# Optimization experiments

Hardware: AMD Instinct MI355X
Metric: run time of the kernel (lower is better)

Reference implementation:

```python
import jax, jax.numpy as jnp
import numpy as np

N_NODES = 20000
N_EDGES = 640000
NODE_DIM = 128
EDGE_DIM = 64
HID = 128  # must equal NODE_DIM (index_add_ into zeros_like(node_feat) in the original)
EPS = 1e-8


def setup_inputs() -> dict:
    key = jax.random.key(0)
    ks = jax.random.split(key, 16)
    s = 0.05
    return {
        "node_feat": jax.random.normal(ks[0], (N_NODES, NODE_DIM), jnp.float32),
        "edge_index": jax.random.randint(ks[1], (2, N_EDGES), 0, N_NODES, jnp.int32),
        "edge_attr": jax.random.normal(ks[2], (N_EDGES, EDGE_DIM), jnp.float32),
        "coords": jax.random.normal(ks[3], (N_NODES, 3), jnp.float32),
        # edge_mlp: Linear(2*node+edge -> hid), SiLU, Linear(hid -> hid), SiLU
        "eW1": jax.random.normal(ks[4], (2 * NODE_DIM + EDGE_DIM, HID), jnp.float32) * s,
        "eb1": jnp.zeros((HID,), jnp.float32),
        "eW2": jax.random.normal(ks[5], (HID, HID), jnp.float32) * s,
        "eb2": jnp.zeros((HID,), jnp.float32),
        # node_mlp: Linear(node+hid -> hid), SiLU, Linear(hid -> node)
        "nW1": jax.random.normal(ks[6], (NODE_DIM + HID, HID), jnp.float32) * s,
        "nb1": jnp.zeros((HID,), jnp.float32),
        "nW2": jax.random.normal(ks[7], (HID, NODE_DIM), jnp.float32) * s,
        "nb2": jnp.zeros((NODE_DIM,), jnp.float32),
        # coord_mlp: Linear(hid -> hid//2), SiLU, Linear(hid//2 -> 1)
        "cW1": jax.random.normal(ks[8], (HID, HID // 2), jnp.float32) * s,
        "cb1": jnp.zeros((HID // 2,), jnp.float32),
        "cW2": jax.random.normal(ks[9], (HID // 2, 1), jnp.float32) * s,
        "cb2": jnp.zeros((1,), jnp.float32),
    }


def reference(node_feat, edge_index, edge_attr, coords,
              eW1, eb1, eW2, eb2, nW1, nb1, nW2, nb2, cW1, cb1, cW2, cb2):
    silu = jax.nn.silu
    src, dst = edge_index[0], edge_index[1]

    # edge messages: gather -> concat -> 2-layer MLP (SiLU after both layers)
    edge_feat = jnp.concatenate([node_feat[src], node_feat[dst], edge_attr], axis=-1)  # [E, 2*node+edge]
    edge_message = silu(silu(edge_feat @ eW1 + eb1) @ eW2 + eb2)  # [E, hid]

    # aggregate messages per destination node (index_add_)
    aggr_message = jax.ops.segment_sum(edge_message, dst, num_segments=N_NODES)  # [N, hid]

    # node update (residual)
    node_input = jnp.concatenate([node_feat, aggr_message], axis=-1)
    node_update = silu(node_input @ nW1 + nb1) @ nW2 + nb2
    updated_nodes = node_feat + node_update

    # coordinate update: per-edge scalar weight times unit direction, scattered to dst
    coord_weights = silu(edge_message @ cW1 + cb1) @ cW2 + cb2  # [E, 1]
    coord_diff = coords[src] - coords[dst]  # [E, 3]
    coord_diff = coord_diff / (jnp.linalg.norm(coord_diff, axis=-1, keepdims=True) + EPS)
    coord_update = jax.ops.segment_sum(coord_weights * coord_diff, dst, num_segments=N_NODES)
    updated_coords = coords + coord_update

    return updated_nodes, updated_coords
```

## Files before the change

kernel.cpp:

```cpp
#include <hip/hip_runtime.h>
#include <math.h>

#define N_NODES 20000
#define N_EDGES 640000
#define D 128
#define ED 64
#define EPS 1e-8f
#define MT 64

#define FSTRIDE 328
#define HSTRIDE 136
#define MSG_OFF (MT * HSTRIDE)
#define LDS_SHORTS (MT * FSTRIDE)

#define NSTRIDE 264

#define EW2_OFF 40960
#define CW1_OFF 57344
#define NW1_OFF 65536
#define NW2_OFF 98304
#define NFBF_OFF 114688
#define CSR_OFF  2674688

typedef __attribute__((ext_vector_type(8))) short bf16x8;
typedef __attribute__((ext_vector_type(4))) short bf16x4;
typedef __attribute__((ext_vector_type(16))) float f32x16;

__device__ __forceinline__ float silu_f(float x) { return x / (1.0f + __expf(-x)); }

__device__ __forceinline__ short f2bf(float f) {
    union { float f; unsigned u; } v; v.f = f;
    unsigned r = v.u + 0x7FFFu + ((v.u >> 16) & 1u);
    return (short)(r >> 16);
}
__device__ __forceinline__ float bf2f(short s) {
    union { unsigned u; float f; } v;
    v.u = ((unsigned)(unsigned short)s) << 16;
    return v.f;
}

#define SWZ_ADD(x, imm) (x + __int_as_float( \
    __builtin_amdgcn_ds_swizzle(__float_as_int(x), imm)))

__global__ __launch_bounds__(256)
void prep_kernel(const float* __restrict__ eW1, const float* __restrict__ eW2,
                 const float* __restrict__ cW1, const float* __restrict__ nW1,
                 const float* __restrict__ nW2,
                 const float* __restrict__ node_feat,
                 const float* __restrict__ coords,
                 short* __restrict__ wsf, short* __restrict__ nfbf,
                 int* __restrict__ cnt,
                 float* __restrict__ nodes_io, float* __restrict__ out_coords) {
    const int t = blockIdx.x * blockDim.x + threadIdx.x;
    const int nthr = gridDim.x * blockDim.x;

    if (t < 224 * 64) {
        int f = t >> 6, lane = t & 63;
        const float* src; int kc, nt, ncol; size_t dst;
        if (f < 80)       {              src = eW1; kc = f >> 2;  nt = f & 3;  ncol = 128; dst = (size_t)f * 512; }
        else if (f < 112) { int g=f-80;  src = eW2; kc = g >> 2;  nt = g & 3;  ncol = 128; dst = EW2_OFF + (size_t)g * 512; }
        else if (f < 128) { int g=f-112; src = cW1; kc = g >> 1;  nt = g & 1;  ncol = 64;  dst = CW1_OFF + (size_t)g * 512; }
        else if (f < 192) { int g=f-128; src = nW1; kc = g >> 2;  nt = g & 3;  ncol = 128; dst = NW1_OFF + (size_t)g * 512; }
        else              { int g=f-192; src = nW2; kc = g >> 2;  nt = g & 3;  ncol = 128; dst = NW2_OFF + (size_t)g * 512; }
        int col = nt * 32 + (lane & 31);
        int k0  = kc * 16 + (lane >> 5) * 8;
        bf16x8 o;
        #pragma unroll
        for (int j = 0; j < 8; ++j) o[j] = f2bf(src[(size_t)(k0 + j) * ncol + col]);
        *(bf16x8*)&wsf[dst + (size_t)lane * 8] = o;
    }
    for (int idx = t; idx < N_NODES * D / 8; idx += nthr) {
        const float* s = node_feat + (size_t)idx * 8;
        float4 f0 = *(const float4*)s, f1 = *(const float4*)(s + 4);
        bf16x8 pk;
        pk[0]=f2bf(f0.x); pk[1]=f2bf(f0.y); pk[2]=f2bf(f0.z); pk[3]=f2bf(f0.w);
        pk[4]=f2bf(f1.x); pk[5]=f2bf(f1.y); pk[6]=f2bf(f1.z); pk[7]=f2bf(f1.w);
        *(bf16x8*)&nfbf[(size_t)idx * 8] = pk;
    }
    for (int idx = t; idx < N_NODES * D / 4; idx += nthr) {
        float4 z; z.x = 0.f; z.y = 0.f; z.z = 0.f; z.w = 0.f;
        *(float4*)&nodes_io[(size_t)idx * 4] = z;
    }
    for (int idx = t; idx < N_NODES; idx += nthr) cnt[idx] = 0;
    for (int idx = t; idx < N_NODES * 3; idx += nthr)
        out_coords[idx] = coords[idx];
}

__global__ __launch_bounds__(256)
void hist_kernel(const int* __restrict__ edge_index, int* __restrict__ cnt) {
    int t = blockIdx.x * blockDim.x + threadIdx.x;
    if (t < N_EDGES) atomicAdd(&cnt[edge_index[N_EDGES + t]], 1);
}

#define SCAN_T 1024
#define SCAN_C 20
__global__ __launch_bounds__(SCAN_T)
void scan_kernel(const int* __restrict__ cnt, int* __restrict__ cursor) {
    __shared__ int part[SCAN_T];
    const int t = threadIdx.x;
    const int base = t * SCAN_C;
    int s = 0;
    #pragma unroll
    for (int i = 0; i < SCAN_C; ++i) {
        int idx = base + i;
        if (idx < N_NODES) s += cnt[idx];
    }
    part[t] = s;
    __syncthreads();
    for (int off = 1; off < SCAN_T; off <<= 1) {
        int v = (t >= off) ? part[t - off] : 0;
        __syncthreads();
        part[t] += v;
        __syncthreads();
    }
    int run = part[t] - s;
    #pragma unroll
    for (int i = 0; i < SCAN_C; ++i) {
        int idx = base + i;
        if (idx < N_NODES) { cursor[idx] = run; run += cnt[idx]; }
    }
}

__global__ __launch_bounds__(256)
void scatter_kernel(const int* __restrict__ edge_index,
                    int* __restrict__ cursor, int* __restrict__ perm) {
    int t = blockIdx.x * blockDim.x + threadIdx.x;
    if (t < N_EDGES) {
        int d = edge_index[N_EDGES + t];
        int pos = atomicAdd(&cursor[d], 1);
        perm[pos] = t;
    }
}

__global__ __launch_bounds__(256, 3)
void edge_kernel(const short* __restrict__ nfbf,
                 const int* __restrict__ edge_index,
                 const int* __restrict__ perm,
                 const float* __restrict__ edge_attr,
                 const float* __restrict__ coords,
                 const float* __restrict__ eb1, const float* __restrict__ eb2,
                 const float* __restrict__ cb1, const float* __restrict__ cW2,
                 const float* __restrict__ cb2,
                 const short* __restrict__ wsf,
                 float* __restrict__ aggr_nodes, float* __restrict__ out_coords) {
    __shared__ __align__(16) short lds[LDS_SHORTS];
    __shared__ int s_src[MT], s_dst[MT];
    __shared__ float s_wgt[MT];
    __shared__ float s_cv[MT][3];
    __shared__ char s_segend[MT];

    const int tid = threadIdx.x;
    const int E0 = blockIdx.x * MT;

    {
        int i = tid >> 2, p = tid & 3;
        int eid  = perm[E0 + i];
        int esrc = edge_index[eid];
        int edst = edge_index[N_EDGES + eid];
        if (p == 0) { s_src[i] = esrc; s_dst[i] = edst; }
        const short* srow = nfbf + (size_t)esrc * D;
        const short* drow = nfbf + (size_t)edst * D;
        short* frow = &lds[i * FSTRIDE];
        #pragma unroll
        for (int c = 0; c < 4; ++c)
            *(bf16x8*)&frow[c * 32 + p * 8] = *(const bf16x8*)&srow[c * 32 + p * 8];
        #pragma unroll
        for (int c = 0; c < 4; ++c)
            *(bf16x8*)&frow[128 + c * 32 + p * 8] = *(const bf16x8*)&drow[c * 32 + p * 8];
        const float* arow = edge_attr + (size_t)eid * ED + p * 16;
        float4 a0 = *(const float4*)&arow[0], a1 = *(const float4*)&arow[4];
        float4 a2 = *(const float4*)&arow[8], a3 = *(const float4*)&arow[12];
        bf16x8 p0, p1;
        p0[0]=f2bf(a0.x); p0[1]=f2bf(a0.y); p0[2]=f2bf(a0.z); p0[3]=f2bf(a0.w);
        p0[4]=f2bf(a1.x); p0[5]=f2bf(a1.y); p0[6]=f2bf(a1.z); p0[7]=f2bf(a1.w);
        p1[0]=f2bf(a2.x); p1[1]=f2bf(a2.y); p1[2]=f2bf(a2.z); p1[3]=f2bf(a2.w);
        p1[4]=f2bf(a3.x); p1[5]=f2bf(a3.y); p1[6]=f2bf(a3.z); p1[7]=f2bf(a3.w);
        *(bf16x8*)&frow[256 + p * 16]     = p0;
        *(bf16x8*)&frow[256 + p * 16 + 8] = p1;
    }
    __syncthreads();

    if (tid < MT)
        s_segend[tid] = (tid == MT - 1) || (s_dst[tid] != s_dst[tid + 1]);

    const int lane  = tid & 63;
    const int wv    = tid >> 6;
    const int m0    = (wv >> 1) * 32;
    const int n0q   = wv & 1;
    const int l31   = lane & 31;
    const int khalf = lane >> 5;

    const bf16x8* W1 = (const bf16x8*)wsf;
    const bf16x8* W2 = (const bf16x8*)(wsf + EW2_OFF);
    const bf16x8* W3 = (const bf16x8*)(wsf + CW1_OFF);

    {
        f32x16 acc0, acc1;
        #pragma unroll
        for (int r = 0; r < 16; ++r) { acc0[r] = 0.f; acc1[r] = 0.f; }
        #pragma unroll
        for (int kc = 0; kc < 20; ++kc) {
            bf16x8 a  = *(const bf16x8*)&lds[(m0 + l31) * FSTRIDE + kc * 16 + khalf * 8];
            bf16x8 b0 = W1[(kc * 4 + n0q * 2 + 0) * 64 + lane];
            bf16x8 b1 = W1[(kc * 4 + n0q * 2 + 1) * 64 + lane];
            acc0 = __builtin_amdgcn_mfma_f32_32x32x16_bf16(a, b0, acc0, 0, 0, 0);
            acc1 = __builtin_amdgcn_mfma_f32_32x32x16_bf16(a, b1, acc1, 0, 0, 0);
        }
        __syncthreads();
        #pragma unroll
        for (int nt = 0; nt < 2; ++nt) {
            f32x16 A = nt ? acc1 : acc0;
            int n = n0q * 64 + nt * 32 + l31;
            float bb = eb1[n];
            #pragma unroll
            for (int r = 0; r < 16; ++r) {
                int row = (r & 3) + 8 * (r >> 2) + 4 * khalf;
                lds[(m0 + row) * HSTRIDE + n] = f2bf(silu_f(A[r] + bb));
            }
        }
    }
    __syncthreads();

    {
        f32x16 acc0, acc1;
        #pragma unroll
        for (int r = 0; r < 16; ++r) { acc0[r] = 0.f; acc1[r] = 0.f; }
        #pragma unroll
        for (int kc = 0; kc < 8; ++kc) {
            bf16x8 a  = *(const bf16x8*)&lds[(m0 + l31) * HSTRIDE + kc * 16 + khalf * 8];
            bf16x8 b0 = W2[(kc * 4 + n0q * 2 + 0) * 64 + lane];
            bf16x8 b1 = W2[(kc * 4 + n0q * 2 + 1) * 64 + lane];
            acc0 = __builtin_amdgcn_mfma_f32_32x32x16_bf16(a, b0, acc0, 0, 0, 0);
            acc1 = __builtin_amdgcn_mfma_f32_32x32x16_bf16(a, b1, acc1, 0, 0, 0);
        }
        #pragma unroll
        for (int nt = 0; nt < 2; ++nt) {
            f32x16 A = nt ? acc1 : acc0;
            int n = n0q * 64 + nt * 32 + l31;
            float bb = eb2[n];
            #pragma unroll
            for (int r = 0; r < 16; ++r) {
                int row = (r & 3) + 8 * (r >> 2) + 4 * khalf;
                lds[MSG_OFF + (m0 + row) * HSTRIDE + n] = f2bf(silu_f(A[r] + bb));
            }
        }
    }
    __syncthreads();

    {
        f32x16 c0, c1;
        #pragma unroll
        for (int r = 0; r < 16; ++r) { c0[r] = 0.f; c1[r] = 0.f; }
        #pragma unroll
        for (int kc = 0; kc < 8; ++kc) {
            bf16x8 a  = *(const bf16x8*)&lds[MSG_OFF + (m0 + l31) * HSTRIDE + kc * 16 + khalf * 8];
            bf16x8 b0 = W3[(kc * 2 + 0) * 64 + lane];
            bf16x8 b1 = W3[(kc * 2 + 1) * 64 + lane];
            c0 = __builtin_amdgcn_mfma_f32_32x32x16_bf16(a, b0, c0, 0, 0, 0);
            c1 = __builtin_amdgcn_mfma_f32_32x32x16_bf16(a, b1, c1, 0, 0, 0);
        }
        float b1a = cb1[l31], b1b = cb1[32 + l31];
        float w2a = cW2[l31], w2b = cW2[32 + l31];
        float part[16];
        #pragma unroll
        for (int r = 0; r < 16; ++r)
            part[r] = silu_f(c0[r] + b1a) * w2a + silu_f(c1[r] + b1b) * w2b;
        #pragma unroll
        for (int r = 0; r < 16; ++r) {
            part[r] = SWZ_ADD(part[r], 0x041F);
            part[r] = SWZ_ADD(part[r], 0x081F);
            part[r] = SWZ_ADD(part[r], 0x101F);
            part[r] = SWZ_ADD(part[r], 0x201F);
            part[r] = SWZ_ADD(part[r], 0x401F);
        }
        if (l31 == 0) {
            float cb2v = cb2[0];
            #pragma unroll
            for (int r = 0; r < 16; ++r)
                s_wgt[m0 + (r & 3) + 8 * (r >> 2) + 4 * khalf] = part[r] + cb2v;
        }
    }
    __syncthreads();

    if (tid < MT) {
        int e = tid;
        float wgt = s_wgt[e];
        int s = s_src[e], d = s_dst[e];
        float dx = coords[s * 3 + 0] - coords[d * 3 + 0];
        float dy = coords[s * 3 + 1] - coords[d * 3 + 1];
        float dz = coords[s * 3 + 2] - coords[d * 3 + 2];
        float inv = wgt / (sqrtf(dx * dx + dy * dy + dz * dz) + EPS);
        s_cv[e][0] = dx * inv; s_cv[e][1] = dy * inv; s_cv[e][2] = dz * inv;
    }
    __syncthreads();

    {
        int q  = tid & 31;
        int st = tid >> 5;
        int c0 = q * 4;
        float a0 = 0.f, a1 = 0.f, a2 = 0.f, a3 = 0.f;
        #pragma unroll
        for (int r = 0; r < 8; ++r) {
            int e = st * 8 + r;
            bf16x4 m = *(const bf16x4*)&lds[MSG_OFF + e * HSTRIDE + c0];
            a0 += bf2f(m[0]); a1 += bf2f(m[1]); a2 += bf2f(m[2]); a3 += bf2f(m[3]);
            if (s_segend[e]) {
                float* ap = &aggr_nodes[(size_t)s_dst[e] * D + c0];
                unsafeAtomicAdd(ap + 0, a0); unsafeAtomicAdd(ap + 1, a1);
                unsafeAtomicAdd(ap + 2, a2); unsafeAtomicAdd(ap + 3, a3);
                a0 = a1 = a2 = a3 = 0.f;
            }
        }
        int elast = st * 8 + 7;
        if (!s_segend[elast]) {
            float* ap = &aggr_nodes[(size_t)s_dst[elast] * D + c0];
            unsafeAtomicAdd(ap + 0, a0); unsafeAtomicAdd(ap + 1, a1);
            unsafeAtomicAdd(ap + 2, a2); unsafeAtomicAdd(ap + 3, a3);
        }
    }

    if (tid < MT) {
        int e = tid;
        bool head = (e == 0) || (s_dst[e] != s_dst[e - 1]);
        if (head) {
            float sx = 0.f, sy = 0.f, sz = 0.f;
            int j = e;
            do {
                sx += s_cv[j][0]; sy += s_cv[j][1]; sz += s_cv[j][2];
                ++j;
            } while (j < MT && s_dst[j] == s_dst[e]);
            int d = s_dst[e];
            unsafeAtomicAdd(&out_coords[d * 3 + 0], sx);
            unsafeAtomicAdd(&out_coords[d * 3 + 1], sy);
            unsafeAtomicAdd(&out_coords[d * 3 + 2], sz);
        }
    }
}

__global__ __launch_bounds__(256, 4)
void node_kernel(const float* __restrict__ node_feat,
                 const short* __restrict__ nfbf,
                 float* nodes_io,
                 const float* __restrict__ nb1, const float* __restrict__ nb2,
                 const short* __restrict__ wsf) {
    __shared__ __align__(16) short lds[MT * NSTRIDE];
    const int tid = threadIdx.x;
    const int N0 = blockIdx.x * MT;

    {
        int i = tid >> 2, p = tid & 3;
        int nid = N0 + i; if (nid > N_NODES - 1) nid = N_NODES - 1;
        const short* frow = nfbf + (size_t)nid * D;
        short* drow = &lds[i * NSTRIDE];
        #pragma unroll
        for (int c = 0; c < 4; ++c)
            *(bf16x8*)&drow[c * 32 + p * 8] = *(const bf16x8*)&frow[c * 32 + p * 8];
        const float* arow = nodes_io + (size_t)nid * D + p * 32;
        #pragma unroll
        for (int c = 0; c < 4; ++c) {
            float4 f0 = *(const float4*)&arow[c * 8];
            float4 f1 = *(const float4*)&arow[c * 8 + 4];
            bf16x8 pk;
            pk[0]=f2bf(f0.x); pk[1]=f2bf(f0.y); pk[2]=f2bf(f0.z); pk[3]=f2bf(f0.w);
            pk[4]=f2bf(f1.x); pk[5]=f2bf(f1.y); pk[6]=f2bf(f1.z); pk[7]=f2bf(f1.w);
            *(bf16x8*)&drow[128 + p * 32 + c * 8] = pk;
        }
    }
    __syncthreads();

    const int lane  = tid & 63;
    const int wv    = tid >> 6;
    const int m0    = (wv >> 1) * 32;
    const int n0q   = wv & 1;
    const int l31   = lane & 31;
    const int khalf = lane >> 5;

    const bf16x8* W1 = (const bf16x8*)(wsf + NW1_OFF);
    const bf16x8* W2 = (const bf16x8*)(wsf + NW2_OFF);

    {
        f32x16 acc0, acc1;
        #pragma unroll
        for (int r = 0; r < 16; ++r) { acc0[r] = 0.f; acc1[r] = 0.f; }
        #pragma unroll
        for (int kc = 0; kc < 16; ++kc) {
            bf16x8 a  = *(const bf16x8*)&lds[(m0 + l31) * NSTRIDE + kc * 16 + khalf * 8];
            bf16x8 b0 = W1[(kc * 4 + n0q * 2 + 0) * 64 + lane];
            bf16x8 b1 = W1[(kc * 4 + n0q * 2 + 1) * 64 + lane];
            acc0 = __builtin_amdgcn_mfma_f32_32x32x16_bf16(a, b0, acc0, 0, 0, 0);
            acc1 = __builtin_amdgcn_mfma_f32_32x32x16_bf16(a, b1, acc1, 0, 0, 0);
        }
        __syncthreads();
        #pragma unroll
        for (int nt = 0; nt < 2; ++nt) {
            f32x16 A = nt ? acc1 : acc0;
            int n = n0q * 64 + nt * 32 + l31;
            float bb = nb1[n];
            #pragma unroll
            for (int r = 0; r < 16; ++r) {
                int row = (r & 3) + 8 * (r >> 2) + 4 * khalf;
                lds[(m0 + row) * HSTRIDE + n] = f2bf(silu_f(A[r] + bb));
            }
        }
    }
    __syncthreads();

    {
        f32x16 acc0, acc1;
        #pragma unroll
        for (int r = 0; r < 16; ++r) { acc0[r] = 0.f; acc1[r] = 0.f; }
        #pragma unroll
        for (int kc = 0; kc < 8; ++kc) {
            bf16x8 a  = *(const bf16x8*)&lds[(m0 + l31) * HSTRIDE + kc * 16 + khalf * 8];
            bf16x8 b0 = W2[(kc * 4 + n0q * 2 + 0) * 64 + lane];
            bf16x8 b1 = W2[(kc * 4 + n0q * 2 + 1) * 64 + lane];
            acc0 = __builtin_amdgcn_mfma_f32_32x32x16_bf16(a, b0, acc0, 0, 0, 0);
            acc1 = __builtin_amdgcn_mfma_f32_32x32x16_bf16(a, b1, acc1, 0, 0, 0);
        }
        #pragma unroll
        for (int nt = 0; nt < 2; ++nt) {
            f32x16 A = nt ? acc1 : acc0;
            int n = n0q * 64 + nt * 32 + l31;
            float bb = nb2[n];
            #pragma unroll
            for (int r = 0; r < 16; ++r) {
                int row = (r & 3) + 8 * (r >> 2) + 4 * khalf;
                int nid = N0 + m0 + row;
                if (nid < N_NODES)
                    nodes_io[(size_t)nid * D + n] = A[r] + bb + node_feat[(size_t)nid * D + n];
            }
        }
    }
}

extern "C" void kernel_launch(void* const* d_in, const int* in_sizes, int n_in,
                              void* d_out, int out_size, void* d_ws, size_t ws_size,
                              hipStream_t stream) {
    const float* node_feat  = (const float*)d_in[0];
    const int*   edge_index = (const int*)d_in[1];
    const float* edge_attr  = (const float*)d_in[2];
    const float* coords     = (const float*)d_in[3];
    const float* eW1 = (const float*)d_in[4];
    const float* eb1 = (const float*)d_in[5];
    const float* eW2 = (const float*)d_in[6];
    const float* eb2 = (const float*)d_in[7];
    const float* nW1 = (const float*)d_in[8];
    const float* nb1 = (const float*)d_in[9];
    const float* nW2 = (const float*)d_in[10];
    const float* nb2 = (const float*)d_in[11];
    const float* cW1 = (const float*)d_in[12];
    const float* cb1 = (const float*)d_in[13];
    const float* cW2 = (const float*)d_in[14];
    const float* cb2 = (const float*)d_in[15];

    float* nodes_io   = (float*)d_out;
    float* out_coords = nodes_io + (size_t)N_NODES * D;
    short* wsf    = (short*)d_ws;
    short* nfbf   = wsf + NFBF_OFF;
    int*   cnt    = (int*)(wsf + CSR_OFF);
    int*   cursor = cnt + N_NODES;
    int*   perm   = cursor + N_NODES;

    prep_kernel<<<256, 256, 0, stream>>>(
        eW1, eW2, cW1, nW1, nW2, node_feat, coords,
        wsf, nfbf, cnt, nodes_io, out_coords);
    hist_kernel<<<N_EDGES / 256, 256, 0, stream>>>(edge_index, cnt);
    scan_kernel<<<1, SCAN_T, 0, stream>>>(cnt, cursor);
    scatter_kernel<<<N_EDGES / 256, 256, 0, stream>>>(edge_index, cursor, perm);
    edge_kernel<<<N_EDGES / MT, 256, 0, stream>>>(
        nfbf, edge_index, perm, edge_attr, coords,
        eb1, eb2, cb1, cW2, cb2, wsf, nodes_io, out_coords);
    node_kernel<<<(N_NODES + MT - 1) / MT, 256, 0, stream>>>(
        node_feat, nfbf, nodes_io, nb1, nb2, wsf);
}
```

Measured before the change: 618.8 us.

## Shrink edge kernel LDS by staging input chunks through one reused buffer

The edge kernel no longer builds the full 328-wide concatenated edge feature tile in LDS. It loads the src rows, dst rows and edge attributes one after another into a single 136-stride buffer, accumulating the first-layer MFMA after each chunk. That buffer is then reused for the hidden and message tiles. The LDS cut is meant to raise occupancy, so launch bounds go from 3 to 6 blocks, at the cost of more barriers and the gather loads being serialized with compute. The scan kernel also stages counts in LDS and writes the cursors with vectorized stores.

```diff
diff --git a/kernel.cpp b/kernel.cpp
--- a/kernel.cpp
+++ b/kernel.cpp
@@ -8,11 +8,8 @@
 #define EPS 1e-8f
 #define MT 64
 
-#define FSTRIDE 328
+#define RSTRIDE 136
 #define HSTRIDE 136
-#define MSG_OFF (MT * HSTRIDE)
-#define LDS_SHORTS (MT * FSTRIDE)
-
 #define NSTRIDE 264
 
 #define EW2_OFF 40960
@@ -96,14 +93,18 @@
 #define SCAN_C 20
 __global__ __launch_bounds__(SCAN_T)
 void scan_kernel(const int* __restrict__ cnt, int* __restrict__ cursor) {
+    __shared__ int lc[N_NODES];
     __shared__ int part[SCAN_T];
     const int t = threadIdx.x;
+    for (int i = t * 4; i < N_NODES; i += SCAN_T * 4)
+        *(int4*)&lc[i] = *(const int4*)&cnt[i];
+    __syncthreads();
     const int base = t * SCAN_C;
     int s = 0;
     #pragma unroll
     for (int i = 0; i < SCAN_C; ++i) {
         int idx = base + i;
-        if (idx < N_NODES) s += cnt[idx];
+        if (idx < N_NODES) s += lc[idx];
     }
     part[t] = s;
     __syncthreads();
@@ -117,8 +118,11 @@
     #pragma unroll
     for (int i = 0; i < SCAN_C; ++i) {
         int idx = base + i;
-        if (idx < N_NODES) { cursor[idx] = run; run += cnt[idx]; }
-    }
+        if (idx < N_NODES) { int c = lc[idx]; lc[idx] = run; run += c; }
+    }
+    __syncthreads();
+    for (int i = t * 4; i < N_NODES; i += SCAN_T * 4)
+        *(int4*)&cursor[i] = *(const int4*)&lc[i];
 }
 
 __global__ __launch_bounds__(256)
@@ -132,7 +136,7 @@
     }
 }
 
-__global__ __launch_bounds__(256, 3)
+__global__ __launch_bounds__(256, 6)
 void edge_kernel(const short* __restrict__ nfbf,
                  const int* __restrict__ edge_index,
                  const int* __restrict__ perm,
@@ -143,7 +147,7 @@
                  const float* __restrict__ cb2,
                  const short* __restrict__ wsf,
                  float* __restrict__ aggr_nodes, float* __restrict__ out_coords) {
-    __shared__ __align__(16) short lds[LDS_SHORTS];
+    __shared__ __align__(16) short R[MT * RSTRIDE];
     __shared__ int s_src[MT], s_dst[MT];
     __shared__ float s_wgt[MT];
     __shared__ float s_cv[MT][3];
@@ -152,21 +156,66 @@
     const int tid = threadIdx.x;
     const int E0 = blockIdx.x * MT;
 
-    {
-        int i = tid >> 2, p = tid & 3;
-        int eid  = perm[E0 + i];
-        int esrc = edge_index[eid];
-        int edst = edge_index[N_EDGES + eid];
-        if (p == 0) { s_src[i] = esrc; s_dst[i] = edst; }
-        const short* srow = nfbf + (size_t)esrc * D;
-        const short* drow = nfbf + (size_t)edst * D;
-        short* frow = &lds[i * FSTRIDE];
+    const int ie = tid >> 2, p = tid & 3;
+    const int eid  = perm[E0 + ie];
+    const int esrc = edge_index[eid];
+    const int edst = edge_index[N_EDGES + eid];
+    if (p == 0) { s_src[ie] = esrc; s_dst[ie] = edst; }
+
+    {
+        const short* row = nfbf + (size_t)esrc * D;
         #pragma unroll
         for (int c = 0; c < 4; ++c)
-            *(bf16x8*)&frow[c * 32 + p * 8] = *(const bf16x8*)&srow[c * 32 + p * 8];
+            *(bf16x8*)&R[ie * RSTRIDE + c * 32 + p * 8] = *(const bf16x8*)&row[c * 32 + p * 8];
+    }
+    __syncthreads();
+    if (tid < MT)
+        s_segend[tid] = (tid == MT - 1) || (s_dst[tid] != s_dst[tid + 1]);
+
+    const int lane  = tid & 63;
+    const int wv    = tid >> 6;
+    const int m0    = (wv >> 1) * 32;
+    const int n0q   = wv & 1;
+    const int l31   = lane & 31;
+    const int khalf = lane >> 5;
+
+    const bf16x8* W1 = (const bf16x8*)wsf;
+    const bf16x8* W2 = (const bf16x8*)(wsf + EW2_OFF);
+    const bf16x8* W3 = (const bf16x8*)(wsf + CW1_OFF);
+
+    f32x16 acc0, acc1;
+    #pragma unroll
+    for (int r = 0; r < 16; ++r) { acc0[r] = 0.f; acc1[r] = 0.f; }
+
+    #pragma unroll
+    for (int kcl = 0; kcl < 8; ++kcl) {
+        bf16x8 a  = *(const bf16x8*)&R[(m0 + l31) * RSTRIDE + kcl * 16 + khalf * 8];
+        bf16x8 b0 = W1[((kcl) * 4 + n0q * 2 + 0) * 64 + lane];
+        bf16x8 b1 = W1[((kcl) * 4 + n0q * 2 + 1) * 64 + lane];
+        acc0 = __builtin_amdgcn_mfma_f32_32x32x16_bf16(a, b0, acc0, 0, 0, 0);
+        acc1 = __builtin_amdgcn_mfma_f32_32x32x16_bf16(a, b1, acc1, 0, 0, 0);
+    }
+    __syncthreads();
+
+    {
+        const short* row = nfbf + (size_t)edst * D;
         #pragma unroll
         for (int c = 0; c < 4; ++c)
-            *(bf16x8*)&frow[128 + c * 32 + p * 8] = *(const bf16x8*)&drow[c * 32 + p * 8];
+            *(bf16x8*)&R[ie * RSTRIDE + c * 32 + p * 8] = *(const bf16x8*)&row[c * 32 + p * 8];
+    }
+    __syncthreads();
+
+    #pragma unroll
+    for (int kcl = 0; kcl < 8; ++kcl) {
+        bf16x8 a  = *(const bf16x8*)&R[(m0 + l31) * RSTRIDE + kcl * 16 + khalf * 8];
+        bf16x8 b0 = W1[((8 + kcl) * 4 + n0q * 2 + 0) * 64 + lane];
+        bf16x8 b1 = W1[((8 + kcl) * 4 + n0q * 2 + 1) * 64 + lane];
+        acc0 = __builtin_amdgcn_mfma_f32_32x32x16_bf16(a, b0, acc0, 0, 0, 0);
+        acc1 = __builtin_amdgcn_mfma_f32_32x32x16_bf16(a, b1, acc1, 0, 0, 0);
+    }
+    __syncthreads();
+
+    {
         const float* arow = edge_attr + (size_t)eid * ED + p * 16;
         float4 a0 = *(const float4*)&arow[0], a1 = *(const float4*)&arow[4];
         float4 a2 = *(const float4*)&arow[8], a3 = *(const float4*)&arow[12];
@@ -175,85 +224,66 @@
         p0[4]=f2bf(a1.x); p0[5]=f2bf(a1.y); p0[6]=f2bf(a1.z); p0[7]=f2bf(a1.w);
         p1[0]=f2bf(a2.x); p1[1]=f2bf(a2.y); p1[2]=f2bf(a2.z); p1[3]=f2bf(a2.w);
         p1[4]=f2bf(a3.x); p1[5]=f2bf(a3.y); p1[6]=f2bf(a3.z); p1[7]=f2bf(a3.w);
-        *(bf16x8*)&frow[256 + p * 16]     = p0;
-        *(bf16x8*)&frow[256 + p * 16 + 8] = p1;
-    }
-    __syncthreads();
-
-    if (tid < MT)
-        s_segend[tid] = (tid == MT - 1) || (s_dst[tid] != s_dst[tid + 1]);
-
-    const int lane  = tid & 63;
-    const int wv    = tid >> 6;
-    const int m0    = (wv >> 1) * 32;
-    const int n0q   = wv & 1;
-    const int l31   = lane & 31;
-    const int khalf = lane >> 5;
-
-    const bf16x8* W1 = (const bf16x8*)wsf;
-    const bf16x8* W2 = (const bf16x8*)(wsf + EW2_OFF);
-    const bf16x8* W3 = (const bf16x8*)(wsf + CW1_OFF);
-
-    {
-        f32x16 acc0, acc1;
-        #pragma unroll
-        for (int r = 0; r < 16; ++r) { acc0[r] = 0.f; acc1[r] = 0.f; }
-        #pragma unroll
-        for (int kc = 0; kc < 20; ++kc) {
-            bf16x8 a  = *(const bf16x8*)&lds[(m0 + l31) * FSTRIDE + kc * 16 + khalf * 8];
-            bf16x8 b0 = W1[(kc * 4 + n0q * 2 + 0) * 64 + lane];
-            bf16x8 b1 = W1[(kc * 4 + n0q * 2 + 1) * 64 + lane];
-            acc0 = __builtin_amdgcn_mfma_f32_32x32x16_bf16(a, b0, acc0, 0, 0, 0);
-            acc1 = __builtin_amdgcn_mfma_f32_32x32x16_bf16(a, b1, acc1, 0, 0, 0);
-        }
-        __syncthreads();
-        #pragma unroll
-        for (int nt = 0; nt < 2; ++nt) {
-            f32x16 A = nt ? acc1 : acc0;
-            int n = n0q * 64 + nt * 32 + l31;
-            float bb = eb1[n];
-            #pragma unroll
-            for (int r = 0; r < 16; ++r) {
-                int row = (r & 3) + 8 * (r >> 2) + 4 * khalf;
-                lds[(m0 + row) * HSTRIDE + n] = f2bf(silu_f(A[r] + bb));
-            }
-        }
-    }
-    __syncthreads();
-
-    {
-        f32x16 acc0, acc1;
-        #pragma unroll
-        for (int r = 0; r < 16; ++r) { acc0[r] = 0.f; acc1[r] = 0.f; }
+        *(bf16x8*)&R[ie * RSTRIDE + p * 16]     = p0;
+        *(bf16x8*)&R[ie * RSTRIDE + p * 16 + 8] = p1;
+    }
+    __syncthreads();
+
+    #pragma unroll
+    for (int kcl = 0; kcl < 4; ++kcl) {
+        bf16x8 a  = *(const bf16x8*)&R[(m0 + l31) * RSTRIDE + kcl * 16 + khalf * 8];
+        bf16x8 b0 = W1[((16 + kcl) * 4 + n0q * 2 + 0) * 64 + lane];
+        bf16x8 b1 = W1[((16 + kcl) * 4 + n0q * 2 + 1) * 64 + lane];
+        acc0 = __builtin_amdgcn_mfma_f32_32x32x16_bf16(a, b0, acc0, 0, 0, 0);
+        acc1 = __builtin_amdgcn_mfma_f32_32x32x16_bf16(a, b1, acc1, 0, 0, 0);
+    }
+    __syncthreads();
+
+    #pragma unroll
+    for (int nt = 0; nt < 2; ++nt) {
+        f32x16 A = nt ? acc1 : acc0;
+        int n = n0q * 64 + nt * 32 + l31;
+        float bb = eb1[n];
+        #pragma unroll
+        for (int r = 0; r < 16; ++r) {
+            int row = (r & 3) + 8 * (r >> 2) + 4 * khalf;
+            R[(m0 + row) * RSTRIDE + n] = f2bf(silu_f(A[r] + bb));
+        }
+    }
+    __syncthreads();
+
+    #pragma unroll
+    for (int r = 0; r < 16; ++r) { acc0[r] = 0.f; acc1[r] = 0.f; }
+    #pragma unroll
+    for (int kc = 0; kc < 8; ++kc) {
+        bf16x8 a  = *(const bf16x8*)&R[(m0 + l31) * RSTRIDE + kc * 16 + khalf * 8];
+        bf16x8 b0 = W2[(kc * 4 + n0q * 2 + 0) * 64 + lane];
+        bf16x8 b1 = W2[(kc * 4 + n0q * 2 + 1) * 64 + lane];
+        acc0 = __builtin_amdgcn_mfma_f32_32x32x16_bf16(a, b0, acc0, 0, 0, 0);
+        acc1 = __builtin_amdgcn_mfma_f32_32x32x16_bf16(a, b1, acc1, 0, 0, 0);
+    }
+    __syncthreads();
+
+    #pragma unroll
+    for (int nt = 0; nt < 2; ++nt) {
+        f32x16 A = nt ? acc1 : acc0;
+        int n = n0q * 64 + nt * 32 + l31;
+        float bb = eb2[n];
+        #pragma unroll
+        for (int r = 0; r < 16; ++r) {
+            int row = (r & 3) + 8 * (r >> 2) + 4 * khalf;
+            R[(m0 + row) * RSTRIDE + n] = f2bf(silu_f(A[r] + bb));
+        }
+    }
+    __syncthreads();
+
+    {
+        f32x16 c0, c1;
+        #pragma unroll
+        for (int r = 0; r < 16; ++r) { c0[r] = 0.f; c1[r] = 0.f; }
         #pragma unroll
         for (int kc = 0; kc < 8; ++kc) {
-            bf16x8 a  = *(const bf16x8*)&lds[(m0 + l31) * HSTRIDE + kc * 16 + khalf * 8];
-            bf16x8 b0 = W2[(kc * 4 + n0q * 2 + 0) * 64 + lane];
-            bf16x8 b1 = W2[(kc * 4 + n0q * 2 + 1) * 64 + lane];
-            acc0 = __builtin_amdgcn_mfma_f32_32x32x16_bf16(a, b0, acc0, 0, 0, 0);
-            acc1 = __builtin_amdgcn_mfma_f32_32x32x16_bf16(a, b1, acc1, 0, 0, 0);
-        }
-        #pragma unroll
-        for (int nt = 0; nt < 2; ++nt) {
-            f32x16 A = nt ? acc1 : acc0;
-            int n = n0q * 64 + nt * 32 + l31;
-            float bb = eb2[n];
-            #pragma unroll
-            for (int r = 0; r < 16; ++r) {
-                int row = (r & 3) + 8 * (r >> 2) + 4 * khalf;
-                lds[MSG_OFF + (m0 + row) * HSTRIDE + n] = f2bf(silu_f(A[r] + bb));
-            }
-        }
-    }
-    __syncthreads();
-
-    {
-        f32x16 c0, c1;
-        #pragma unroll
-        for (int r = 0; r < 16; ++r) { c0[r] = 0.f; c1[r] = 0.f; }
-        #pragma unroll
-        for (int kc = 0; kc < 8; ++kc) {
-            bf16x8 a  = *(const bf16x8*)&lds[MSG_OFF + (m0 + l31) * HSTRIDE + kc * 16 + khalf * 8];
+            bf16x8 a  = *(const bf16x8*)&R[(m0 + l31) * RSTRIDE + kc * 16 + khalf * 8];
             bf16x8 b0 = W3[(kc * 2 + 0) * 64 + lane];
             bf16x8 b1 = W3[(kc * 2 + 1) * 64 + lane];
             c0 = __builtin_amdgcn_mfma_f32_32x32x16_bf16(a, b0, c0, 0, 0, 0);
@@ -302,7 +332,7 @@
         #pragma unroll
         for (int r = 0; r < 8; ++r) {
             int e = st * 8 + r;
-            bf16x4 m = *(const bf16x4*)&lds[MSG_OFF + e * HSTRIDE + c0];
+            bf16x4 m = *(const bf16x4*)&R[e * RSTRIDE + c0];
             a0 += bf2f(m[0]); a1 += bf2f(m[1]); a2 += bf2f(m[2]); a3 += bf2f(m[3]);
             if (s_segend[e]) {
                 float* ap = &aggr_nodes[(size_t)s_dst[e] * D + c0];
```

Measured after the change: 609.2 us. Within noise of the previous version (-1.5%).
